# Optimization experiments

Measured on AMD Instinct MI355X. Metric: run time of the kernel, lower is better.

The kernel has to match this reference:

```python
import jax, jax.numpy as jnp
import numpy as np

B, S, D = 2, 2048, 512
E, K = 8, 2
H = 4 * D  # expert_dim
EPS = 1e-10


def setup_inputs() -> dict:
    key = jax.random.key(0)
    ks = jax.random.split(key, 5)
    scale = 1.0 / np.sqrt(D)
    return {
        "x": jax.random.normal(ks[0], (B, S, D), dtype=jnp.float32),
        "w_router": jax.random.normal(ks[1], (D, E), dtype=jnp.float32) * scale,
        "w_gate": jax.random.normal(ks[2], (D, E * H), dtype=jnp.float32) * scale,
        "w_up": jax.random.normal(ks[3], (D, E * H), dtype=jnp.float32) * scale,
        "w_down": jax.random.normal(ks[4], (H, D), dtype=jnp.float32) * (1.0 / np.sqrt(H)),
    }


def reference(x, w_router, w_gate, w_up, w_down):
    b, s, d = x.shape
    n = b * s
    xf = x.reshape(n, d)

    # Router: softmax over experts, pick top-k, renormalize
    router_probs = jax.nn.softmax(xf @ w_router, axis=-1)          # [N, E]
    top_p, top_i = jax.lax.top_k(router_probs, K)                  # [N, K]
    top_p = top_p / (top_p.sum(axis=-1, keepdims=True) + EPS)

    # Dense all-expert gate/up projections (as in original module)
    gate = jax.nn.silu(xf @ w_gate).reshape(n, E, H)               # [N, E, H]
    up = (xf @ w_up).reshape(n, E, H)                              # [N, E, H]

    # Gather per-token top-k expert slices and combine
    sel_gate = jnp.take_along_axis(gate, top_i[:, :, None], axis=1)  # [N, K, H]
    sel_up = jnp.take_along_axis(up, top_i[:, :, None], axis=1)      # [N, K, H]
    combined = jnp.sum(top_p[:, :, None] * sel_gate * sel_up, axis=1)  # [N, H]

    out = (combined @ w_down).reshape(b, s, d)

    # Load-balancing aux loss
    expert_probs = router_probs.mean(axis=0)                       # [E]
    lb_loss = E * jnp.sum(expert_probs * jnp.log(expert_probs * E + EPS))
    return out, lb_loss
```

## Files before the change

kernel.cpp:

```cpp
#include <hip/hip_runtime.h>
#include <hip/hip_bf16.h>

#define N_TOK 4096
#define D_DIM 512
#define E_NUM 8
#define H_DIM 2048
#define RB_NUM 256
#define TP_NUM 8704

typedef __attribute__((ext_vector_type(8))) short short8;
typedef __attribute__((ext_vector_type(4))) float f32x4;

__device__ inline short f2bs(float f) {
  __hip_bfloat16 h = __float2bfloat16(f);
  return *reinterpret_cast<short*>(&h);
}

__device__ inline void llds16(const short* g, short* l) {
  __builtin_amdgcn_global_load_lds(
      (const __attribute__((address_space(1))) void*)g,
      (__attribute__((address_space(3))) void*)l, 16, 0, 0);
}

__device__ inline void pipeb() {
  asm volatile("s_waitcnt vmcnt(0)" ::: "memory");
  __builtin_amdgcn_s_barrier();
}

__global__ void __launch_bounds__(256) prep_router_kernel(
    const float* __restrict__ wg, const float* __restrict__ wu,
    const float* __restrict__ wd, const float* __restrict__ x,
    const float* __restrict__ wr, short* __restrict__ wgb,
    short* __restrict__ wub, short* __restrict__ wdb, short* __restrict__ xb,
    int* __restrict__ cnt_blk, int* __restrict__ tok_bkt,
    float* __restrict__ p_bkt, float* __restrict__ psum_blk) {
  int u = blockIdx.x;
  int tid = threadIdx.x;

  if (u >= RB_NUM) {
    __shared__ float tbuf[64][33];
    int v = u - RB_NUM;
    const float* in;
    short* op;
    int R, C, c0, r0;
    if (v < 8192) {
      in = (v < 4096) ? wg : wu;
      op = (v < 4096) ? wgb : wub;
      int w = v & 4095;
      R = D_DIM; C = E_NUM * H_DIM;
      c0 = (w & 511) * 32; r0 = (w >> 9) * 64;
    } else {
      in = wd; op = wdb;
      int w = v - 8192;
      R = H_DIM; C = D_DIM;
      c0 = (w & 15) * 32; r0 = (w >> 4) * 64;
    }
    int tx = tid & 31, ty = tid >> 5;
#pragma unroll
    for (int i = 0; i < 8; ++i)
      tbuf[ty + 8 * i][tx] = in[(size_t)(r0 + ty + 8 * i) * C + c0 + tx];
    __syncthreads();
#pragma unroll
    for (int i = 0; i < 4; ++i) {
      int cl = ty + 8 * i;
      unsigned lo = (unsigned short)f2bs(tbuf[2 * tx][cl]);
      unsigned hi = (unsigned short)f2bs(tbuf[2 * tx + 1][cl]);
      ((int*)op)[(((size_t)(c0 + cl) * R) + r0) / 2 + tx] = (int)(lo | (hi << 16));
    }
    return;
  }

  __shared__ float wr_t[E_NUM * D_DIM];
  __shared__ int h_cnt[E_NUM];
  __shared__ float psh[E_NUM];
  int rb = u;
  for (int i = tid; i < D_DIM * E_NUM; i += 256)
    wr_t[(i & 7) * D_DIM + (i >> 3)] = wr[i];
  if (tid < E_NUM) { h_cnt[tid] = 0; psh[tid] = 0.f; }
  __syncthreads();

  int r = tid >> 4, pp = tid & 15;
  int t = rb * 16 + r;
  const float* xr0 = x + (size_t)t * D_DIM;
  short* xw0 = xb + (size_t)t * D_DIM;
  float acc[8] = {0, 0, 0, 0, 0, 0, 0, 0};
#pragma unroll
  for (int j = 0; j < 8; ++j) {
    int d = j * 64 + pp * 4;
    float4 xv = *(const float4*)(xr0 + d);
    short4 o;
    o.x = f2bs(xv.x); o.y = f2bs(xv.y); o.z = f2bs(xv.z); o.w = f2bs(xv.w);
    *(short4*)(xw0 + d) = o;
#pragma unroll
    for (int e = 0; e < 8; ++e) {
      float4 w = *(const float4*)&wr_t[e * D_DIM + d];
      acc[e] += xv.x * w.x + xv.y * w.y + xv.z * w.z + xv.w * w.w;
    }
  }
#pragma unroll
  for (int e = 0; e < 8; ++e) {
    acc[e] += __shfl_xor(acc[e], 1);
    acc[e] += __shfl_xor(acc[e], 2);
    acc[e] += __shfl_xor(acc[e], 4);
    acc[e] += __shfl_xor(acc[e], 8);
  }

  if (pp == 0) {
    float m = acc[0];
#pragma unroll
    for (int e = 1; e < 8; ++e) m = fmaxf(m, acc[e]);
    float p[8], s = 0.f;
#pragma unroll
    for (int e = 0; e < 8; ++e) { p[e] = expf(acc[e] - m); s += p[e]; }
    float inv = 1.f / s;
#pragma unroll
    for (int e = 0; e < 8; ++e) {
      p[e] *= inv;
      atomicAdd(&psh[e], p[e]);
    }
    int i0 = 0;
#pragma unroll
    for (int e = 1; e < 8; ++e) if (p[e] > p[i0]) i0 = e;
    int i1 = (i0 == 0) ? 1 : 0;
#pragma unroll
    for (int e = 0; e < 8; ++e) if (e != i0 && p[e] > p[i1]) i1 = e;
    float ps = p[i0] + p[i1] + 1e-10f;
    float q0 = p[i0] / ps, q1 = p[i1] / ps;
    int l0 = atomicAdd(&h_cnt[i0], 1);
    int l1 = atomicAdd(&h_cnt[i1], 1);
    tok_bkt[i0 * (RB_NUM * 16) + rb * 16 + l0] = t * 2 + 0;
    p_bkt[i0 * (RB_NUM * 16) + rb * 16 + l0] = q0;
    tok_bkt[i1 * (RB_NUM * 16) + rb * 16 + l1] = t * 2 + 1;
    p_bkt[i1 * (RB_NUM * 16) + rb * 16 + l1] = q1;
  }
  __syncthreads();
  if (tid < E_NUM) {
    cnt_blk[rb * 8 + tid] = h_cnt[tid];
    psum_blk[rb * 8 + tid] = psh[tid];
  }
}

__global__ void __launch_bounds__(256, 1) moe_gateup_kernel(
    const short* __restrict__ xb, const short* __restrict__ wg,
    const short* __restrict__ wu, const int* __restrict__ cnt_blk,
    const int* __restrict__ tok_bkt, const float* __restrict__ p_bkt,
    const float* __restrict__ psum_blk, short* __restrict__ act,
    float* __restrict__ out_loss) {
  int e = blockIdx.z;
  int tid = threadIdx.x;

  if (e == 8) {
    if (blockIdx.x || blockIdx.y) return;
    __shared__ float sums[8];
    if (tid < 8) sums[tid] = 0.f;
    __syncthreads();
#pragma unroll
    for (int ee = 0; ee < 8; ++ee)
      atomicAdd(&sums[ee], psum_blk[tid * 8 + ee]);
    __syncthreads();
    if (tid == 0) {
      float lb = 0.f;
#pragma unroll
      for (int ee = 0; ee < 8; ++ee) {
        float pe = sums[ee] / (float)N_TOK;
        lb += pe * logf(pe * 8.f + 1e-10f);
      }
      out_loss[0] = 8.f * lb;
    }
    return;
  }

  __shared__ __align__(16) short As[2][256 * 64];
  __shared__ __align__(16) short Bgs[2][64 * 64];
  __shared__ __align__(16) short Bus[2][64 * 64];
  __shared__ int scan[256];
  __shared__ int wsum[4];
  __shared__ int s_row[256];
  __shared__ float s_pr[256];

  int lane = tid & 63, wid = tid >> 6;

  {
    int c = cnt_blk[tid * 8 + e];
#pragma unroll
    for (int ofs = 1; ofs < 64; ofs <<= 1) {
      int v = __shfl_up(c, ofs);
      if (lane >= ofs) c += v;
    }
    if (lane == 63) wsum[wid] = c;
    __syncthreads();
    int pre = 0;
#pragma unroll
    for (int w = 0; w < 4; ++w) pre += (w < wid) ? wsum[w] : 0;
    scan[tid] = c + pre;
    __syncthreads();
  }
  int n_e = scan[255];
  int rt = blockIdx.y;
  if (rt * 256 >= n_e) return;
  int h0 = blockIdx.x * 64;

  {
    int r = rt * 256 + tid;
    int srow = -1;
    float spr = 0.f;
    if (r < n_e) {
      int lo = 0, hi = 255;
      while (lo < hi) { int mid = (lo + hi) >> 1; if (scan[mid] > r) hi = mid; else lo = mid + 1; }
      int prev = lo ? scan[lo - 1] : 0;
      int idx = e * (RB_NUM * 16) + lo * 16 + (r - prev);
      srow = tok_bkt[idx];
      spr = p_bkt[idx];
    }
    s_row[tid] = srow;
    s_pr[tid] = spr;
  }
  __syncthreads();

  int cg = (lane & 7) ^ (lane >> 3);
  const short* baseA[8];
  const short* baseB[4];
#pragma unroll
  for (int jj = 0; jj < 8; ++jj) {
    int r = wid * 64 + jj * 8 + (lane >> 3);
    int row = s_row[r];
    int t = (row < 0) ? 0 : (row >> 1);
    baseA[jj] = xb + (size_t)t * D_DIM + cg * 8;
  }
  int ldsB_off = (wid & 1) * 2048;
  short* ldsBbase = (wid & 2) ? &Bus[0][0] : &Bgs[0][0];
  {
    const short* wB = ((wid & 2) ? wu : wg) + (size_t)e * H_DIM * D_DIM;
    int rb = (wid & 1) * 32;
#pragma unroll
    for (int jj = 0; jj < 4; ++jj) {
      int h = h0 + rb + jj * 8 + (lane >> 3);
      baseB[jj] = wB + (size_t)h * D_DIM + cg * 8;
    }
  }

  int ml = lane & 15, quad = lane >> 4;
  int m0w = wid * 64;
  f32x4 accG[4][4], accU[4][4];
#pragma unroll
  for (int mf = 0; mf < 4; ++mf)
#pragma unroll
    for (int nf = 0; nf < 4; ++nf) {
      accG[mf][nf] = (f32x4){0, 0, 0, 0};
      accU[mf][nf] = (f32x4){0, 0, 0, 0};
    }

  auto stage = [&](int bi, int kt) {
    int kb = kt * 64;
#pragma unroll
    for (int jj = 0; jj < 8; ++jj)
      llds16(baseA[jj] + kb, &As[bi][wid * 4096 + jj * 512]);
#pragma unroll
    for (int jj = 0; jj < 4; ++jj)
      llds16(baseB[jj] + kb, ldsBbase + bi * 4096 + ldsB_off + jj * 512);
  };

  auto compute = [&](int cur) {
#pragma unroll
    for (int ks = 0; ks < 2; ++ks) {
      int cs = ((quad + ks * 4) ^ (ml & 7)) * 8;
      short8 a[4], bg[4], bu[4];
#pragma unroll
      for (int mf = 0; mf < 4; ++mf)
        a[mf] = *(const short8*)&As[cur][(m0w + mf * 16 + ml) * 64 + cs];
#pragma unroll
      for (int nf = 0; nf < 4; ++nf) {
        bg[nf] = *(const short8*)&Bgs[cur][(nf * 16 + ml) * 64 + cs];
        bu[nf] = *(const short8*)&Bus[cur][(nf * 16 + ml) * 64 + cs];
      }
#pragma unroll
      for (int mf = 0; mf < 4; ++mf)
#pragma unroll
        for (int nf = 0; nf < 4; ++nf) {
          accG[mf][nf] = __builtin_amdgcn_mfma_f32_16x16x32_bf16(a[mf], bg[nf], accG[mf][nf], 0, 0, 0);
          accU[mf][nf] = __builtin_amdgcn_mfma_f32_16x16x32_bf16(a[mf], bu[nf], accU[mf][nf], 0, 0, 0);
        }
    }
  };

  stage(0, 0);
  pipeb();
#pragma unroll
  for (int kt = 0; kt < 7; ++kt) {
    stage((kt + 1) & 1, kt + 1);
    compute(kt & 1);
    pipeb();
  }
  compute(1);

#pragma unroll
  for (int mf = 0; mf < 4; ++mf)
#pragma unroll
    for (int r = 0; r < 4; ++r) {
      int rl = m0w + mf * 16 + quad * 4 + r;
      int arow = s_row[rl];
      if (arow >= 0) {
        float pr = s_pr[rl];
#pragma unroll
        for (int nf = 0; nf < 4; ++nf) {
          float g = accG[mf][nf][r], u = accU[mf][nf][r];
          float val = pr * (g / (1.f + __expf(-g))) * u;
          act[(size_t)arow * H_DIM + h0 + nf * 16 + ml] = f2bs(val);
        }
      }
    }
}

__global__ void __launch_bounds__(256, 2) down_kernel(
    const short* __restrict__ act, const short* __restrict__ wd,
    float* __restrict__ out) {
  __shared__ __align__(16) short As[2][2][128 * 64];
  __shared__ __align__(16) short Bs[2][64 * 64];
  int d0 = blockIdx.x * 64;
  int t0 = blockIdx.y * 128;
  int tid = threadIdx.x, lane = tid & 63, wid = tid >> 6;
  int cg = (lane & 7) ^ (lane >> 3);

  const short* baseA[4];
  const short* baseB[2];
#pragma unroll
  for (int jj = 0; jj < 4; ++jj) {
    int r = wid * 32 + jj * 8 + (lane >> 3);
    baseA[jj] = act + (size_t)(2 * (t0 + r)) * H_DIM + cg * 8;
  }
#pragma unroll
  for (int jj = 0; jj < 2; ++jj) {
    int d = d0 + wid * 16 + jj * 8 + (lane >> 3);
    baseB[jj] = wd + (size_t)d * H_DIM + cg * 8;
  }

  int ml = lane & 15, quad = lane >> 4;
  f32x4 acc[2][4];
#pragma unroll
  for (int mf = 0; mf < 2; ++mf)
#pragma unroll
    for (int nf = 0; nf < 4; ++nf) acc[mf][nf] = (f32x4){0, 0, 0, 0};

  auto stage = [&](int bi, int j) {
    int hb = j * 64;
#pragma unroll
    for (int s = 0; s < 2; ++s)
#pragma unroll
      for (int jj = 0; jj < 4; ++jj)
        llds16(baseA[jj] + (size_t)s * H_DIM + hb, &As[bi][s][wid * 2048 + jj * 512]);
#pragma unroll
    for (int jj = 0; jj < 2; ++jj)
      llds16(baseB[jj] + hb, &Bs[bi][(wid * 16 + jj * 8) * 64]);
  };

  auto compute = [&](int bi) {
#pragma unroll
    for (int ks = 0; ks < 2; ++ks) {
      int cs = ((quad + ks * 4) ^ (ml & 7)) * 8;
      short8 b[4];
#pragma unroll
      for (int nf = 0; nf < 4; ++nf)
        b[nf] = *(const short8*)&Bs[bi][(nf * 16 + ml) * 64 + cs];
#pragma unroll
      for (int s = 0; s < 2; ++s) {
        short8 a[2];
#pragma unroll
        for (int mf = 0; mf < 2; ++mf)
          a[mf] = *(const short8*)&As[bi][s][(wid * 32 + mf * 16 + ml) * 64 + cs];
#pragma unroll
        for (int mf = 0; mf < 2; ++mf)
#pragma unroll
          for (int nf = 0; nf < 4; ++nf)
            acc[mf][nf] = __builtin_amdgcn_mfma_f32_16x16x32_bf16(a[mf], b[nf], acc[mf][nf], 0, 0, 0);
      }
    }
  };

  stage(0, 0);
  pipeb();
#pragma unroll 2
  for (int j = 0; j < 31; ++j) {
    stage((j + 1) & 1, j + 1);
    compute(j & 1);
    pipeb();
  }
  compute(1);

#pragma unroll
  for (int mf = 0; mf < 2; ++mf)
#pragma unroll
    for (int r = 0; r < 4; ++r) {
      int t = t0 + wid * 32 + mf * 16 + quad * 4 + r;
#pragma unroll
      for (int nf = 0; nf < 4; ++nf)
        out[(size_t)t * D_DIM + d0 + nf * 16 + ml] = acc[mf][nf][r];
    }
}

extern "C" void kernel_launch(void* const* d_in, const int* in_sizes, int n_in,
                              void* d_out, int out_size, void* d_ws, size_t ws_size,
                              hipStream_t stream) {
  const float* x = (const float*)d_in[0];
  const float* wr = (const float*)d_in[1];
  const float* wg = (const float*)d_in[2];
  const float* wu = (const float*)d_in[3];
  const float* wd = (const float*)d_in[4];
  float* out = (float*)d_out;

  char* ws = (char*)d_ws;
  size_t off = 0;
  auto alloc = [&](size_t bytes) {
    char* p = ws + off;
    off += (bytes + 255) & ~(size_t)255;
    return p;
  };
  short* xb = (short*)alloc((size_t)N_TOK * D_DIM * 2);
  short* wgb = (short*)alloc((size_t)E_NUM * H_DIM * D_DIM * 2);
  short* wub = (short*)alloc((size_t)E_NUM * H_DIM * D_DIM * 2);
  short* wdb = (short*)alloc((size_t)D_DIM * H_DIM * 2);
  short* act = (short*)alloc((size_t)N_TOK * 2 * H_DIM * 2);
  int* cnt_blk = (int*)alloc((size_t)RB_NUM * E_NUM * 4);
  int* tok_bkt = (int*)alloc((size_t)E_NUM * RB_NUM * 16 * 4);
  float* p_bkt = (float*)alloc((size_t)E_NUM * RB_NUM * 16 * 4);
  float* psum_blk = (float*)alloc((size_t)RB_NUM * E_NUM * 4);

  prep_router_kernel<<<RB_NUM + TP_NUM, 256, 0, stream>>>(
      wg, wu, wd, x, wr, wgb, wub, wdb, xb, cnt_blk, tok_bkt, p_bkt, psum_blk);
  moe_gateup_kernel<<<dim3(H_DIM / 64, N_TOK / 256, E_NUM + 1), 256, 0, stream>>>(
      xb, wgb, wub, cnt_blk, tok_bkt, p_bkt, psum_blk, act,
      out + (size_t)N_TOK * D_DIM);
  down_kernel<<<dim3(D_DIM / 64, N_TOK / 128), 256, 0, stream>>>(act, wdb, out);
}
```

Measured before the change: 247.4 us.

## Shrink gate-up row tile and split down GEMM over top-k slots with reduction

The gate/up kernel's token tile drops from 256 to 128 rows, with launch bounds raised to two blocks per CU. This reduces LDS and register use and wastes fewer rows on per-expert padding. The down projection now computes each top-k slot separately with larger 128x128 output tiles and a remapped block order, writing two fp32 partial buffers. A new reduce kernel sums those partials. This adds an extra launch and extra global memory traffic for the partials in exchange for better MFMA reuse and parallelism.

Result: faster. 234.4 us (-5.3%).

```diff
diff --git a/kernel.cpp b/kernel.cpp
--- a/kernel.cpp
+++ b/kernel.cpp
@@ -140,7 +140,7 @@
   }
 }
 
-__global__ void __launch_bounds__(256, 1) moe_gateup_kernel(
+__global__ void __launch_bounds__(256, 2) moe_gateup_kernel(
     const short* __restrict__ xb, const short* __restrict__ wg,
     const short* __restrict__ wu, const int* __restrict__ cnt_blk,
     const int* __restrict__ tok_bkt, const float* __restrict__ p_bkt,
@@ -170,13 +170,13 @@
     return;
   }
 
-  __shared__ __align__(16) short As[2][256 * 64];
+  __shared__ __align__(16) short As[2][128 * 64];
   __shared__ __align__(16) short Bgs[2][64 * 64];
   __shared__ __align__(16) short Bus[2][64 * 64];
   __shared__ int scan[256];
   __shared__ int wsum[4];
-  __shared__ int s_row[256];
-  __shared__ float s_pr[256];
+  __shared__ int s_row[128];
+  __shared__ float s_pr[128];
 
   int lane = tid & 63, wid = tid >> 6;
 
@@ -197,11 +197,11 @@
   }
   int n_e = scan[255];
   int rt = blockIdx.y;
-  if (rt * 256 >= n_e) return;
+  if (rt * 128 >= n_e) return;
   int h0 = blockIdx.x * 64;
 
-  {
-    int r = rt * 256 + tid;
+  if (tid < 128) {
+    int r = rt * 128 + tid;
     int srow = -1;
     float spr = 0.f;
     if (r < n_e) {
@@ -218,11 +218,11 @@
   __syncthreads();
 
   int cg = (lane & 7) ^ (lane >> 3);
-  const short* baseA[8];
+  const short* baseA[4];
   const short* baseB[4];
 #pragma unroll
-  for (int jj = 0; jj < 8; ++jj) {
-    int r = wid * 64 + jj * 8 + (lane >> 3);
+  for (int jj = 0; jj < 4; ++jj) {
+    int r = wid * 32 + jj * 8 + (lane >> 3);
     int row = s_row[r];
     int t = (row < 0) ? 0 : (row >> 1);
     baseA[jj] = xb + (size_t)t * D_DIM + cg * 8;
@@ -240,10 +240,10 @@
   }
 
   int ml = lane & 15, quad = lane >> 4;
-  int m0w = wid * 64;
-  f32x4 accG[4][4], accU[4][4];
-#pragma unroll
-  for (int mf = 0; mf < 4; ++mf)
+  int m0w = wid * 32;
+  f32x4 accG[2][4], accU[2][4];
+#pragma unroll
+  for (int mf = 0; mf < 2; ++mf)
 #pragma unroll
     for (int nf = 0; nf < 4; ++nf) {
       accG[mf][nf] = (f32x4){0, 0, 0, 0};
@@ -253,8 +253,8 @@
   auto stage = [&](int bi, int kt) {
     int kb = kt * 64;
 #pragma unroll
-    for (int jj = 0; jj < 8; ++jj)
-      llds16(baseA[jj] + kb, &As[bi][wid * 4096 + jj * 512]);
+    for (int jj = 0; jj < 4; ++jj)
+      llds16(baseA[jj] + kb, &As[bi][wid * 2048 + jj * 512]);
 #pragma unroll
     for (int jj = 0; jj < 4; ++jj)
       llds16(baseB[jj] + kb, ldsBbase + bi * 4096 + ldsB_off + jj * 512);
@@ -264,9 +264,9 @@
 #pragma unroll
     for (int ks = 0; ks < 2; ++ks) {
       int cs = ((quad + ks * 4) ^ (ml & 7)) * 8;
-      short8 a[4], bg[4], bu[4];
-#pragma unroll
-      for (int mf = 0; mf < 4; ++mf)
+      short8 a[2], bg[4], bu[4];
+#pragma unroll
+      for (int mf = 0; mf < 2; ++mf)
         a[mf] = *(const short8*)&As[cur][(m0w + mf * 16 + ml) * 64 + cs];
 #pragma unroll
       for (int nf = 0; nf < 4; ++nf) {
@@ -274,7 +274,7 @@
         bu[nf] = *(const short8*)&Bus[cur][(nf * 16 + ml) * 64 + cs];
       }
 #pragma unroll
-      for (int mf = 0; mf < 4; ++mf)
+      for (int mf = 0; mf < 2; ++mf)
 #pragma unroll
         for (int nf = 0; nf < 4; ++nf) {
           accG[mf][nf] = __builtin_amdgcn_mfma_f32_16x16x32_bf16(a[mf], bg[nf], accG[mf][nf], 0, 0, 0);
@@ -294,7 +294,7 @@
   compute(1);
 
 #pragma unroll
-  for (int mf = 0; mf < 4; ++mf)
+  for (int mf = 0; mf < 2; ++mf)
 #pragma unroll
     for (int r = 0; r < 4; ++r) {
       int rl = m0w + mf * 16 + quad * 4 + r;
@@ -313,66 +313,63 @@
 
 __global__ void __launch_bounds__(256, 2) down_kernel(
     const short* __restrict__ act, const short* __restrict__ wd,
-    float* __restrict__ out) {
-  __shared__ __align__(16) short As[2][2][128 * 64];
-  __shared__ __align__(16) short Bs[2][64 * 64];
-  int d0 = blockIdx.x * 64;
-  int t0 = blockIdx.y * 128;
+    float* __restrict__ partial) {
+  int bid = blockIdx.x;
+  int w = (bid & 7) * 32 + (bid >> 3);
+  int z = w >> 7;
+  int y = (w >> 2) & 31;
+  int xk = w & 3;
+  int d0 = xk * 128;
+  int t0 = y * 128;
+
+  __shared__ __align__(16) short As[2][128 * 64];
+  __shared__ __align__(16) short Bs[2][128 * 64];
   int tid = threadIdx.x, lane = tid & 63, wid = tid >> 6;
   int cg = (lane & 7) ^ (lane >> 3);
 
   const short* baseA[4];
-  const short* baseB[2];
+  const short* baseB[4];
 #pragma unroll
   for (int jj = 0; jj < 4; ++jj) {
     int r = wid * 32 + jj * 8 + (lane >> 3);
-    baseA[jj] = act + (size_t)(2 * (t0 + r)) * H_DIM + cg * 8;
-  }
-#pragma unroll
-  for (int jj = 0; jj < 2; ++jj) {
-    int d = d0 + wid * 16 + jj * 8 + (lane >> 3);
+    baseA[jj] = act + (size_t)(2 * (t0 + r) + z) * H_DIM + cg * 8;
+    int d = d0 + wid * 32 + jj * 8 + (lane >> 3);
     baseB[jj] = wd + (size_t)d * H_DIM + cg * 8;
   }
 
   int ml = lane & 15, quad = lane >> 4;
-  f32x4 acc[2][4];
-#pragma unroll
-  for (int mf = 0; mf < 2; ++mf)
+  int m0w = (wid & 1) * 64, n0w = (wid >> 1) * 64;
+  f32x4 acc[4][4];
+#pragma unroll
+  for (int mf = 0; mf < 4; ++mf)
 #pragma unroll
     for (int nf = 0; nf < 4; ++nf) acc[mf][nf] = (f32x4){0, 0, 0, 0};
 
   auto stage = [&](int bi, int j) {
     int hb = j * 64;
 #pragma unroll
-    for (int s = 0; s < 2; ++s)
-#pragma unroll
-      for (int jj = 0; jj < 4; ++jj)
-        llds16(baseA[jj] + (size_t)s * H_DIM + hb, &As[bi][s][wid * 2048 + jj * 512]);
-#pragma unroll
-    for (int jj = 0; jj < 2; ++jj)
-      llds16(baseB[jj] + hb, &Bs[bi][(wid * 16 + jj * 8) * 64]);
+    for (int jj = 0; jj < 4; ++jj) {
+      llds16(baseA[jj] + hb, &As[bi][wid * 2048 + jj * 512]);
+      llds16(baseB[jj] + hb, &Bs[bi][wid * 2048 + jj * 512]);
+    }
   };
 
   auto compute = [&](int bi) {
 #pragma unroll
     for (int ks = 0; ks < 2; ++ks) {
       int cs = ((quad + ks * 4) ^ (ml & 7)) * 8;
-      short8 b[4];
+      short8 a[4], b[4];
+#pragma unroll
+      for (int mf = 0; mf < 4; ++mf)
+        a[mf] = *(const short8*)&As[bi][(m0w + mf * 16 + ml) * 64 + cs];
 #pragma unroll
       for (int nf = 0; nf < 4; ++nf)
-        b[nf] = *(const short8*)&Bs[bi][(nf * 16 + ml) * 64 + cs];
-#pragma unroll
-      for (int s = 0; s < 2; ++s) {
-        short8 a[2];
-#pragma unroll
-        for (int mf = 0; mf < 2; ++mf)
-          a[mf] = *(const short8*)&As[bi][s][(wid * 32 + mf * 16 + ml) * 64 + cs];
-#pragma unroll
-        for (int mf = 0; mf < 2; ++mf)
-#pragma unroll
-          for (int nf = 0; nf < 4; ++nf)
-            acc[mf][nf] = __builtin_amdgcn_mfma_f32_16x16x32_bf16(a[mf], b[nf], acc[mf][nf], 0, 0, 0);
-      }
+        b[nf] = *(const short8*)&Bs[bi][(n0w + nf * 16 + ml) * 64 + cs];
+#pragma unroll
+      for (int mf = 0; mf < 4; ++mf)
+#pragma unroll
+        for (int nf = 0; nf < 4; ++nf)
+          acc[mf][nf] = __builtin_amdgcn_mfma_f32_16x16x32_bf16(a[mf], b[nf], acc[mf][nf], 0, 0, 0);
     }
   };
 
@@ -386,15 +383,26 @@
   }
   compute(1);
 
-#pragma unroll
-  for (int mf = 0; mf < 2; ++mf)
+  float* pout = partial + (size_t)z * N_TOK * D_DIM;
+#pragma unroll
+  for (int mf = 0; mf < 4; ++mf)
 #pragma unroll
     for (int r = 0; r < 4; ++r) {
-      int t = t0 + wid * 32 + mf * 16 + quad * 4 + r;
+      int t = t0 + m0w + mf * 16 + quad * 4 + r;
 #pragma unroll
       for (int nf = 0; nf < 4; ++nf)
-        out[(size_t)t * D_DIM + d0 + nf * 16 + ml] = acc[mf][nf][r];
-    }
+        pout[(size_t)t * D_DIM + d0 + n0w + nf * 16 + ml] = acc[mf][nf][r];
+    }
+}
+
+__global__ void __launch_bounds__(256) reduce_kernel(
+    const float* __restrict__ partial, float* __restrict__ out) {
+  int i = blockIdx.x * 256 + threadIdx.x;
+  const int Q = N_TOK * D_DIM / 4;
+  const float4* p = (const float4*)partial;
+  float4 a = p[i], b = p[i + Q];
+  float4 r = {a.x + b.x, a.y + b.y, a.z + b.z, a.w + b.w};
+  ((float4*)out)[i] = r;
 }
 
 extern "C" void kernel_launch(void* const* d_in, const int* in_sizes, int n_in,
@@ -419,6 +427,7 @@
   short* wub = (short*)alloc((size_t)E_NUM * H_DIM * D_DIM * 2);
   short* wdb = (short*)alloc((size_t)D_DIM * H_DIM * 2);
   short* act = (short*)alloc((size_t)N_TOK * 2 * H_DIM * 2);
+  float* partial = (float*)alloc((size_t)2 * N_TOK * D_DIM * 4);
   int* cnt_blk = (int*)alloc((size_t)RB_NUM * E_NUM * 4);
   int* tok_bkt = (int*)alloc((size_t)E_NUM * RB_NUM * 16 * 4);
   float* p_bkt = (float*)alloc((size_t)E_NUM * RB_NUM * 16 * 4);
@@ -426,8 +435,9 @@
 
   prep_router_kernel<<<RB_NUM + TP_NUM, 256, 0, stream>>>(
       wg, wu, wd, x, wr, wgb, wub, wdb, xb, cnt_blk, tok_bkt, p_bkt, psum_blk);
-  moe_gateup_kernel<<<dim3(H_DIM / 64, N_TOK / 256, E_NUM + 1), 256, 0, stream>>>(
+  moe_gateup_kernel<<<dim3(H_DIM / 64, N_TOK / 128, E_NUM + 1), 256, 0, stream>>>(
       xb, wgb, wub, cnt_blk, tok_bkt, p_bkt, psum_blk, act,
       out + (size_t)N_TOK * D_DIM);
-  down_kernel<<<dim3(D_DIM / 64, N_TOK / 128), 256, 0, stream>>>(act, wdb, out);
-}
+  down_kernel<<<256, 256, 0, stream>>>(act, wdb, partial);
+  reduce_kernel<<<N_TOK * D_DIM / 4 / 256, 256, 0, stream>>>(partial, out);
+}
```
